# Kernel optimization log

Hardware: AMD Instinct MI355X
Metric: run time of the kernel (lower is better)

## Reference

```python
import jax, jax.numpy as jnp
import numpy as np

NUM_HEADS = 16
WINDOW = 256


def setup_inputs() -> dict:
    key = jax.random.key(0)
    ks = jax.random.split(key, 9)
    B, S, E = 2, 2048, 1024
    sc = 1.0 / np.sqrt(E)
    return {
        "x": jax.random.normal(ks[0], (B, S, E), dtype=jnp.float32),
        "Wq": jax.random.normal(ks[1], (E, E), dtype=jnp.float32) * sc,
        "bq": jnp.zeros((E,), dtype=jnp.float32),
        "Wk": jax.random.normal(ks[2], (E, E), dtype=jnp.float32) * sc,
        "bk": jnp.zeros((E,), dtype=jnp.float32),
        "Wv": jax.random.normal(ks[3], (E, E), dtype=jnp.float32) * sc,
        "bv": jnp.zeros((E,), dtype=jnp.float32),
        "Wo": jax.random.normal(ks[4], (E, E), dtype=jnp.float32) * sc,
        "bo": jnp.zeros((E,), dtype=jnp.float32),
    }


def reference(x, Wq, bq, Wk, bk, Wv, bv, Wo, bo):
    B, S, E = x.shape
    H = NUM_HEADS
    D = E // H
    Q = (x @ Wq + bq).reshape(B, S, H, D).transpose(0, 2, 1, 3)  # [B,H,S,D]
    # Faithful to original: K is view(B, H, S, D), NOT a permute of (B,S,H,D)
    K = (x @ Wk + bk).reshape(B, H, S, D)
    V = (x @ Wv + bv).reshape(B, S, H, D).transpose(0, 2, 1, 3)  # [B,H,S,D]
    scores = jnp.einsum('bhqd,bhkd->bhqk', Q, K) / jnp.sqrt(jnp.float32(D))
    # sliding-window mask: j in [i-W, i+W)  (diag included, i+W exclusive)
    i = jnp.arange(S)[:, None]
    j = jnp.arange(S)[None, :]
    mask = (j >= i - WINDOW) & (j < i + WINDOW)  # [S,S]
    scores = jnp.where(mask, scores, -jnp.inf)
    attn = jax.nn.softmax(scores, axis=-1)
    out = jnp.einsum('bhqk,bhkd->bhqd', attn, V)  # [B,H,S,D]
    out = out.transpose(0, 2, 1, 3).reshape(B, S, E)
    return out @ Wo + bo
```

## Files before the change

kernel.cpp:

```cpp
#include <hip/hip_runtime.h>

#define S_LEN 2048
#define EMB   1024
#define HEADS 16
#define HDIM  64
#define WIN   256

typedef unsigned short u16;
typedef unsigned int   u32;
typedef float  f32x4  __attribute__((ext_vector_type(4)));
typedef __bf16 bf16x8 __attribute__((ext_vector_type(8)));
typedef unsigned short u16x4 __attribute__((ext_vector_type(4)));

typedef const __attribute__((address_space(1))) u32* gas_ptr;
typedef __attribute__((address_space(3))) u32*       las_ptr;

__device__ __forceinline__ void gload16(const void* g, void* l) {
    __builtin_amdgcn_global_load_lds((gas_ptr)g, (las_ptr)l, 16, 0, 0);
}

__device__ __forceinline__ u16 f2bf(float v) {
    u32 x = __builtin_bit_cast(u32, v);
    return (u16)((x + 0x7fffu + ((x >> 16) & 1u)) >> 16);
}
__device__ __forceinline__ u32 cvt_pk_bf16(float lo, float hi) {
    u32 r;
    asm volatile("v_cvt_pk_bf16_f32 %0, %1, %2" : "=v"(r) : "v"(lo), "v"(hi));
    return r;
}

__global__ __launch_bounds__(256)
void prep_kernel(const float* __restrict__ W0, const float* __restrict__ W1,
                 const float* __restrict__ W2, const float* __restrict__ W3,
                 u16* __restrict__ T0, u16* __restrict__ T1,
                 u16* __restrict__ T2, u16* __restrict__ T3,
                 const float* __restrict__ x, u16* __restrict__ xh, int n4)
{
    const int z = blockIdx.z;
    const int tid = threadIdx.x;

    if (z == 4) {
        int bid = blockIdx.x + 16 * blockIdx.y;
        for (int i = bid * 256 + tid; i < n4; i += 65536) {
            float4 v = reinterpret_cast<const float4*>(x)[i];
            u16x4 o;
            o[0] = f2bf(v.x); o[1] = f2bf(v.y); o[2] = f2bf(v.z); o[3] = f2bf(v.w);
            reinterpret_cast<u16x4*>(xh)[i] = o;
        }
        return;
    }

    const float* W = (z == 0) ? W0 : (z == 1) ? W1 : (z == 2) ? W2 : W3;
    u16* T = (z == 0) ? T0 : (z == 1) ? T1 : (z == 2) ? T2 : T3;

    __shared__ float Ts[64][68];
    const int k0 = blockIdx.x * 64, n0 = blockIdx.y * 64;

    int r = tid >> 2, c0 = (tid & 3) * 16;
#pragma unroll
    for (int q = 0; q < 4; ++q) {
        float4 v = *reinterpret_cast<const float4*>(W + (size_t)(k0 + r) * EMB + n0 + c0 + 4 * q);
        *reinterpret_cast<float4*>(&Ts[r][c0 + 4 * q]) = v;
    }
    __syncthreads();

    int n = tid >> 2, kk0 = (tid & 3) * 16;
    u16 hb[16];
#pragma unroll
    for (int e = 0; e < 16; ++e) hb[e] = f2bf(Ts[kk0 + e][n]);
    size_t base = (size_t)(n0 + n) * EMB + k0 + kk0;
#pragma unroll
    for (int q = 0; q < 2; ++q) {
        u32 w[4];
#pragma unroll
        for (int e = 0; e < 4; ++e)
            w[e] = (u32)hb[q * 8 + 2 * e] | ((u32)hb[q * 8 + 2 * e + 1] << 16);
        *reinterpret_cast<uint4*>(T + base + q * 8) = make_uint4(w[0], w[1], w[2], w[3]);
    }
}

template<int NFN, bool OUTBF>
__global__ __launch_bounds__(256, 3)
void mfma_gemm(const u16* __restrict__ A,
               const u16* __restrict__ B0, const u16* __restrict__ B1,
               const u16* __restrict__ B2,
               const float* __restrict__ bias0, const float* __restrict__ bias1,
               const float* __restrict__ bias2,
               float s0, float s1, float s2,
               void* __restrict__ Y0, void* __restrict__ Y1, void* __restrict__ Y2,
               int M, int N, int K)
{
    constexpr int TNB = NFN * 32;

    const int z = blockIdx.z;
    const u16*   Bt   = (z == 0) ? B0 : (z == 1) ? B1 : B2;
    const float* bias = (z == 0) ? bias0 : (z == 1) ? bias1 : bias2;
    const float  scl  = (z == 0) ? s0 : (z == 1) ? s1 : s2;
    void*        Y    = (z == 0) ? Y0 : (z == 1) ? Y1 : Y2;

    __shared__ u16 lds[(128 + TNB) * 64];
    u16* lA = lds;
    u16* lB = lds + 128 * 64;

    const int tid  = threadIdx.x;
    const int wid  = tid >> 6, lane = tid & 63;
    const int wr   = wid >> 1, wc = wid & 1;
    const int lr   = lane & 15, lg = lane >> 4;
    const int l7   = lr & 7;
    const int bm   = blockIdx.y * 128, bn = blockIdx.x * TNB;

    const int crow = lane >> 3;
    const int cgrp = (lane & 7) ^ crow;

    f32x4 acc[4][NFN];
#pragma unroll
    for (int i = 0; i < 4; ++i)
#pragma unroll
        for (int j = 0; j < NFN; ++j) acc[i][j] = (f32x4)0.0f;

    for (int k0 = 0; k0 < K; k0 += 64) {
#pragma unroll
        for (int q = 0; q < 4; ++q) {
            int ch = wid * 4 + q;
            gload16(A + (size_t)(bm + ch * 8 + crow) * K + k0 + cgrp * 8,
                    lA + ch * 512);
        }
#pragma unroll
        for (int q = 0; q < TNB / 32; ++q) {
            int ch = wid * (TNB / 32) + q;
            gload16(Bt + (size_t)(bn + ch * 8 + crow) * K + k0 + cgrp * 8,
                    lB + ch * 512);
        }
        __syncthreads();

#pragma unroll
        for (int ks = 0; ks < 2; ++ks) {
            const int gsw = ((ks * 4 + lg) ^ l7) << 3;
            bf16x8 a0[4], b0[NFN];
#pragma unroll
            for (int mf = 0; mf < 4; ++mf)
                a0[mf] = *reinterpret_cast<const bf16x8*>(
                    lA + (wr * 64 + mf * 16 + lr) * 64 + gsw);
#pragma unroll
            for (int nf = 0; nf < NFN; ++nf)
                b0[nf] = *reinterpret_cast<const bf16x8*>(
                    lB + (wc * NFN * 16 + nf * 16 + lr) * 64 + gsw);
#pragma unroll
            for (int mf = 0; mf < 4; ++mf)
#pragma unroll
                for (int nf = 0; nf < NFN; ++nf)
                    acc[mf][nf] = __builtin_amdgcn_mfma_f32_16x16x32_bf16(
                        a0[mf], b0[nf], acc[mf][nf], 0, 0, 0);
        }
        __syncthreads();
    }

#pragma unroll
    for (int nf = 0; nf < NFN; ++nf) {
        int col = bn + wc * NFN * 16 + nf * 16 + lr;
        float bs = bias[col];
#pragma unroll
        for (int mf = 0; mf < 4; ++mf) {
#pragma unroll
            for (int r = 0; r < 4; ++r) {
                int row = bm + wr * 64 + mf * 16 + lg * 4 + r;
                float val = (acc[mf][nf][r] + bs) * scl;
                if (OUTBF)
                    ((u16*)Y)[(size_t)row * N + col] = f2bf(val);
                else
                    ((float*)Y)[(size_t)row * N + col] = val;
            }
        }
    }
}

__global__ __launch_bounds__(512, 4)
void attn_mfma_kernel(const u16* __restrict__ Qb, const u16* __restrict__ Kb,
                      const u16* __restrict__ Vb, u16* __restrict__ AOh)
{
    __shared__ u16 Ks[2][64 * 64];
    __shared__ u16 Vt[2][64 * 64];
    __shared__ u16 Ps[8 * 16 * 64];

    constexpr float L2E = 1.44269504f;

    const int nwg = gridDim.x * gridDim.y * gridDim.z;
    int n  = blockIdx.x + gridDim.x * (blockIdx.y + gridDim.y * blockIdx.z);
    int sw = (n & 7) * (nwg >> 3) + (n >> 3);
    const int qb = sw & 15;
    const int h  = (sw >> 4) & 15;
    const int b  = sw >> 8;

    const int i0  = qb * 128;
    const int tid = threadIdx.x;
    const int wid = tid >> 6, lane = tid & 63;
    const int lr  = lane & 15, lg = lane >> 4;
    const int l7  = lr & 7;

    const u16* Kh = Kb + (size_t)b * S_LEN * EMB + (size_t)h * S_LEN * HDIM;

    bf16x8 qa[2];
    {
        const u16* qp = Qb + ((size_t)(b * S_LEN + i0 + wid * 16 + lr)) * EMB
                        + h * HDIM + lg * 8;
        qa[0] = *reinterpret_cast<const bf16x8*>(qp);
        qa[1] = *reinterpret_cast<const bf16x8*>(qp + 32);
    }

    float m2 = -1e30f, l = 0.0f;
    f32x4 o[4];
#pragma unroll
    for (int nf = 0; nf < 4; ++nf) o[nf] = (f32x4)0.0f;

    const int tlo = (2 * qb < 4) ? 0 : 2 * qb - 4;
    const int thi = (2 * qb + 5 > 31) ? 31 : 2 * qb + 5;
    const int qg  = i0 + wid * 16 + lr;

    const int kj   = lane >> 3;
    const int kgsw = (lane & 7) ^ kj;

    const int vjp = (tid & 31) * 2, vdc = tid >> 5;
    const u16* Vh = Vb + (size_t)b * S_LEN * EMB + h * HDIM;

    uint2 vr0 = *reinterpret_cast<const uint2*>(Vh + (size_t)(tlo * 64 + vjp) * EMB + vdc * 4);
    uint2 vr1 = *reinterpret_cast<const uint2*>(Vh + (size_t)(tlo * 64 + vjp + 1) * EMB + vdc * 4);
    gload16(Kh + (size_t)(tlo * 64 + wid * 8 + kj) * HDIM + kgsw * 8,
            Ks[0] + wid * 512);

    int cur = 0;
    for (int t = tlo; t <= thi; ++t) {
        {
            const u16* e0 = reinterpret_cast<const u16*>(&vr0);
            const u16* e1 = reinterpret_cast<const u16*>(&vr1);
            int jg = vjp >> 3, jl = vjp & 7;
#pragma unroll
            for (int e = 0; e < 4; ++e) {
                int d = vdc * 4 + e;
                u32 w = (u32)e0[e] | ((u32)e1[e] << 16);
                *reinterpret_cast<u32*>(Vt[cur] + d * 64 + ((jg ^ (d & 7)) << 3) + jl) = w;
            }
        }
        __syncthreads();

        if (t < thi) {
            gload16(Kh + (size_t)((t + 1) * 64 + wid * 8 + kj) * HDIM + kgsw * 8,
                    Ks[cur ^ 1] + wid * 512);
            vr0 = *reinterpret_cast<const uint2*>(Vh + (size_t)((t + 1) * 64 + vjp) * EMB + vdc * 4);
            vr1 = *reinterpret_cast<const uint2*>(Vh + (size_t)((t + 1) * 64 + vjp + 1) * EMB + vdc * 4);
        }

        f32x4 s[4];
#pragma unroll
        for (int nf = 0; nf < 4; ++nf) s[nf] = (f32x4)0.0f;
#pragma unroll
        for (int ks = 0; ks < 2; ++ks) {
            int cg = (ks * 4 + lg) ^ l7;
#pragma unroll
            for (int nf = 0; nf < 4; ++nf) {
                bf16x8 kf = *reinterpret_cast<const bf16x8*>(
                    Ks[cur] + (nf * 16 + lr) * 64 + (cg << 3));
                s[nf] = __builtin_amdgcn_mfma_f32_16x16x32_bf16(kf, qa[ks], s[nf], 0, 0, 0);
            }
        }

        if (t <= 2 * qb - 3 || t >= 2 * qb + 4) {
            int klo = qg - WIN, khi = qg + WIN;
#pragma unroll
            for (int nf = 0; nf < 4; ++nf) {
#pragma unroll
                for (int r = 0; r < 4; ++r) {
                    int kg = t * 64 + nf * 16 + lg * 4 + r;
                    bool ok = (kg >= klo) && (kg < khi);
                    s[nf][r] = ok ? s[nf][r] : -1e30f;
                }
            }
        }

        float tmax = s[0][0];
#pragma unroll
        for (int nf = 0; nf < 4; ++nf)
#pragma unroll
            for (int r = 0; r < 4; ++r) tmax = fmaxf(tmax, s[nf][r]);
        tmax = fmaxf(tmax, __shfl_xor(tmax, 16));
        tmax = fmaxf(tmax, __shfl_xor(tmax, 32));
        float tmax2 = tmax * L2E;

        bool need = tmax2 > m2 + 12.0f;
        if (__any(need)) {
            float mn2 = fmaxf(m2, tmax2);
            float sc = __builtin_amdgcn_exp2f(m2 - mn2);
            m2 = mn2;
            l *= sc;
#pragma unroll
            for (int r = 0; r < 4; ++r) {
                float scr = __shfl(sc, lg * 4 + r);
#pragma unroll
                for (int nf = 0; nf < 4; ++nf) o[nf][r] *= scr;
            }
        }

        float ps = 0.0f;
#pragma unroll
        for (int nf = 0; nf < 4; ++nf) {
            float p0 = __builtin_amdgcn_exp2f(fmaf(s[nf][0], L2E, -m2));
            float p1 = __builtin_amdgcn_exp2f(fmaf(s[nf][1], L2E, -m2));
            float p2 = __builtin_amdgcn_exp2f(fmaf(s[nf][2], L2E, -m2));
            float p3 = __builtin_amdgcn_exp2f(fmaf(s[nf][3], L2E, -m2));
            ps += (p0 + p1) + (p2 + p3);
            u32 pk0 = cvt_pk_bf16(p0, p1);
            u32 pk1 = cvt_pk_bf16(p2, p3);
            int idx16 = wid * 1024 + lr * 64 +
                        (((nf * 2 + (lg >> 1)) ^ l7) << 3) + (lg & 1) * 4;
            *reinterpret_cast<uint2*>(Ps + idx16) = make_uint2(pk0, pk1);
        }
        ps += __shfl_xor(ps, 16);
        ps += __shfl_xor(ps, 32);
        l += ps;

#pragma unroll
        for (int ks = 0; ks < 2; ++ks) {
            int cg = (ks * 4 + lg) ^ l7;
            bf16x8 pf = *reinterpret_cast<const bf16x8*>(
                Ps + wid * 1024 + lr * 64 + (cg << 3));
#pragma unroll
            for (int nf = 0; nf < 4; ++nf) {
                bf16x8 vf = *reinterpret_cast<const bf16x8*>(
                    Vt[cur] + (nf * 16 + lr) * 64 + (cg << 3));
                o[nf] = __builtin_amdgcn_mfma_f32_16x16x32_bf16(pf, vf, o[nf], 0, 0, 0);
            }
        }
        cur ^= 1;
    }

    float inv = 1.0f / l;
#pragma unroll
    for (int r = 0; r < 4; ++r) {
        float invr = __shfl(inv, lg * 4 + r);
#pragma unroll
        for (int nf = 0; nf < 4; ++nf) {
            size_t idx = ((size_t)(b * S_LEN + i0 + wid * 16 + lg * 4 + r)) * EMB
                         + h * HDIM + nf * 16 + lr;
            AOh[idx] = f2bf(o[nf][r] * invr);
        }
    }
}

extern "C" void kernel_launch(void* const* d_in, const int* in_sizes, int n_in,
                              void* d_out, int out_size, void* d_ws, size_t ws_size,
                              hipStream_t stream)
{
    (void)n_in; (void)out_size; (void)ws_size;
    const float* x  = (const float*)d_in[0];
    const float* Wq = (const float*)d_in[1];
    const float* bq = (const float*)d_in[2];
    const float* Wk = (const float*)d_in[3];
    const float* bk = (const float*)d_in[4];
    const float* Wv = (const float*)d_in[5];
    const float* bv = (const float*)d_in[6];
    const float* Wo = (const float*)d_in[7];
    const float* bo = (const float*)d_in[8];
    float* out = (float*)d_out;

    const int B = in_sizes[0] / (S_LEN * EMB);
    const int M = B * S_LEN;

    u16* xh  = (u16*)d_ws;
    u16* WtQ = xh  + (size_t)M * EMB;
    u16* WtK = WtQ + (size_t)EMB * EMB;
    u16* WtV = WtK + (size_t)EMB * EMB;
    u16* WtO = WtV + (size_t)EMB * EMB;
    u16* Qb  = WtO + (size_t)EMB * EMB;
    u16* Kb  = Qb + (size_t)M * EMB;
    u16* Vb  = Kb + (size_t)M * EMB;
    u16* AOh = Vb + (size_t)M * EMB;

    int n4 = M * EMB / 4;
    dim3 gt(EMB / 64, EMB / 64, 5);
    prep_kernel<<<gt, 256, 0, stream>>>(Wq, Wk, Wv, Wo, WtQ, WtK, WtV, WtO,
                                        x, xh, n4);

    dim3 g1(EMB / 128, M / 128, 3);
    mfma_gemm<4, true><<<g1, 256, 0, stream>>>(
        xh, WtQ, WtK, WtV, bq, bk, bv, 0.125f, 1.0f, 1.0f,
        Qb, Kb, Vb, M, EMB, EMB);

    dim3 g2(S_LEN / 128, HEADS, B);
    attn_mfma_kernel<<<g2, 512, 0, stream>>>(Qb, Kb, Vb, AOh);

    dim3 g3(EMB / 64, M / 128, 1);
    mfma_gemm<2, false><<<g3, 256, 0, stream>>>(
        AOh, WtO, WtO, WtO, bo, bo, bo, 1.0f, 1.0f, 1.0f,
        out, out, out, M, EMB, EMB);
}
```

Baseline: 87.77 us.

## Widen QKV GEMM tile to 128x256 and process key tiles in pairs in attention

The QKV projection GEMM now uses a 128x256 output tile with 8 N-fragments per wave and an occupancy hint of 2, instead of 128x128 with a hint of 3. This raises A-tile reuse and MFMA density per LDS load but uses more registers and LDS. The attention kernel now stages two 64-key tiles per barrier using doubled K/V LDS buffers, which halves the number of __syncthreads and lengthens prefetch distance. The output GEMM is specialized into its own non-template kernel without behaviour change. The tile count is always even (6 or 10), so the pairing is valid.

```diff
diff --git a/kernel.cpp b/kernel.cpp
--- a/kernel.cpp
+++ b/kernel.cpp
@@ -79,24 +79,104 @@
     }
 }
 
-template<int NFN, bool OUTBF>
-__global__ __launch_bounds__(256, 3)
-void mfma_gemm(const u16* __restrict__ A,
-               const u16* __restrict__ B0, const u16* __restrict__ B1,
-               const u16* __restrict__ B2,
-               const float* __restrict__ bias0, const float* __restrict__ bias1,
-               const float* __restrict__ bias2,
-               float s0, float s1, float s2,
-               void* __restrict__ Y0, void* __restrict__ Y1, void* __restrict__ Y2,
-               int M, int N, int K)
+__global__ __launch_bounds__(256, 2)
+void mfma_gemm_qkv(const u16* __restrict__ A,
+                   const u16* __restrict__ B0, const u16* __restrict__ B1,
+                   const u16* __restrict__ B2,
+                   const float* __restrict__ bias0, const float* __restrict__ bias1,
+                   const float* __restrict__ bias2,
+                   float s0, float s1, float s2,
+                   u16* __restrict__ Y0, u16* __restrict__ Y1, u16* __restrict__ Y2,
+                   int M, int N, int K)
 {
-    constexpr int TNB = NFN * 32;
-
     const int z = blockIdx.z;
     const u16*   Bt   = (z == 0) ? B0 : (z == 1) ? B1 : B2;
     const float* bias = (z == 0) ? bias0 : (z == 1) ? bias1 : bias2;
     const float  scl  = (z == 0) ? s0 : (z == 1) ? s1 : s2;
-    void*        Y    = (z == 0) ? Y0 : (z == 1) ? Y1 : Y2;
+    u16*         Y    = (z == 0) ? Y0 : (z == 1) ? Y1 : Y2;
+
+    __shared__ u16 lds[(128 + 256) * 64];
+    u16* lA = lds;
+    u16* lB = lds + 128 * 64;
+
+    const int tid  = threadIdx.x;
+    const int wid  = tid >> 6, lane = tid & 63;
+    const int wr   = wid >> 1, wc = wid & 1;
+    const int lr   = lane & 15, lg = lane >> 4;
+    const int l7   = lr & 7;
+    const int bm   = blockIdx.y * 128, bn = blockIdx.x * 256;
+
+    const int crow = lane >> 3;
+    const int cgrp = (lane & 7) ^ crow;
+
+    f32x4 acc[4][8];
+#pragma unroll
+    for (int i = 0; i < 4; ++i)
+#pragma unroll
+        for (int j = 0; j < 8; ++j) acc[i][j] = (f32x4)0.0f;
+
+    for (int k0 = 0; k0 < K; k0 += 64) {
+#pragma unroll
+        for (int q = 0; q < 4; ++q) {
+            int ch = wid * 4 + q;
+            gload16(A + (size_t)(bm + ch * 8 + crow) * K + k0 + cgrp * 8,
+                    lA + ch * 512);
+        }
+#pragma unroll
+        for (int q = 0; q < 8; ++q) {
+            int ch = wid * 8 + q;
+            gload16(Bt + (size_t)(bn + ch * 8 + crow) * K + k0 + cgrp * 8,
+                    lB + ch * 512);
+        }
+        __syncthreads();
+
+#pragma unroll
+        for (int ks = 0; ks < 2; ++ks) {
+            const int gsw = ((ks * 4 + lg) ^ l7) << 3;
+            bf16x8 a0[4];
+#pragma unroll
+            for (int mf = 0; mf < 4; ++mf)
+                a0[mf] = *reinterpret_cast<const bf16x8*>(
+                    lA + (wr * 64 + mf * 16 + lr) * 64 + gsw);
+#pragma unroll
+            for (int half = 0; half < 2; ++half) {
+                bf16x8 b0[4];
+#pragma unroll
+                for (int j = 0; j < 4; ++j)
+                    b0[j] = *reinterpret_cast<const bf16x8*>(
+                        lB + (wc * 128 + (half * 4 + j) * 16 + lr) * 64 + gsw);
+#pragma unroll
+                for (int mf = 0; mf < 4; ++mf)
+#pragma unroll
+                    for (int j = 0; j < 4; ++j)
+                        acc[mf][half * 4 + j] = __builtin_amdgcn_mfma_f32_16x16x32_bf16(
+                            a0[mf], b0[j], acc[mf][half * 4 + j], 0, 0, 0);
+            }
+        }
+        __syncthreads();
+    }
+
+#pragma unroll
+    for (int nf = 0; nf < 8; ++nf) {
+        int col = bn + wc * 128 + nf * 16 + lr;
+        float bs = bias[col];
+#pragma unroll
+        for (int mf = 0; mf < 4; ++mf) {
+#pragma unroll
+            for (int r = 0; r < 4; ++r) {
+                int row = bm + wr * 64 + mf * 16 + lg * 4 + r;
+                Y[(size_t)row * N + col] = f2bf((acc[mf][nf][r] + bs) * scl);
+            }
+        }
+    }
+}
+
+__global__ __launch_bounds__(256, 3)
+void mfma_gemm_o(const u16* __restrict__ A, const u16* __restrict__ Bt,
+                 const float* __restrict__ bias, float* __restrict__ Y,
+                 int M, int N, int K)
+{
+    constexpr int TNB = 64;
 
     __shared__ u16 lds[(128 + TNB) * 64];
     u16* lA = lds;
@@ -112,11 +192,11 @@
     const int crow = lane >> 3;
     const int cgrp = (lane & 7) ^ crow;
 
-    f32x4 acc[4][NFN];
+    f32x4 acc[4][2];
 #pragma unroll
     for (int i = 0; i < 4; ++i)
 #pragma unroll
-        for (int j = 0; j < NFN; ++j) acc[i][j] = (f32x4)0.0f;
+        for (int j = 0; j < 2; ++j) acc[i][j] = (f32x4)0.0f;
 
     for (int k0 = 0; k0 < K; k0 += 64) {
 #pragma unroll
@@ -126,8 +206,8 @@
                     lA + ch * 512);
         }
 #pragma unroll
-        for (int q = 0; q < TNB / 32; ++q) {
-            int ch = wid * (TNB / 32) + q;
+        for (int q = 0; q < 2; ++q) {
+            int ch = wid * 2 + q;
             gload16(Bt + (size_t)(bn + ch * 8 + crow) * K + k0 + cgrp * 8,
                     lB + ch * 512);
         }
@@ -136,19 +216,19 @@
 #pragma unroll
         for (int ks = 0; ks < 2; ++ks) {
             const int gsw = ((ks * 4 + lg) ^ l7) << 3;
-            bf16x8 a0[4], b0[NFN];
+            bf16x8 a0[4], b0[2];
 #pragma unroll
             for (int mf = 0; mf < 4; ++mf)
                 a0[mf] = *reinterpret_cast<const bf16x8*>(
                     lA + (wr * 64 + mf * 16 + lr) * 64 + gsw);
 #pragma unroll
-            for (int nf = 0; nf < NFN; ++nf)
+            for (int nf = 0; nf < 2; ++nf)
                 b0[nf] = *reinterpret_cast<const bf16x8*>(
-                    lB + (wc * NFN * 16 + nf * 16 + lr) * 64 + gsw);
+                    lB + (wc * 32 + nf * 16 + lr) * 64 + gsw);
 #pragma unroll
             for (int mf = 0; mf < 4; ++mf)
 #pragma unroll
-                for (int nf = 0; nf < NFN; ++nf)
+                for (int nf = 0; nf < 2; ++nf)
                     acc[mf][nf] = __builtin_amdgcn_mfma_f32_16x16x32_bf16(
                         a0[mf], b0[nf], acc[mf][nf], 0, 0, 0);
         }
@@ -156,19 +236,15 @@
     }
 
 #pragma unroll
-    for (int nf = 0; nf < NFN; ++nf) {
-        int col = bn + wc * NFN * 16 + nf * 16 + lr;
+    for (int nf = 0; nf < 2; ++nf) {
+        int col = bn + wc * 32 + nf * 16 + lr;
         float bs = bias[col];
 #pragma unroll
         for (int mf = 0; mf < 4; ++mf) {
 #pragma unroll
             for (int r = 0; r < 4; ++r) {
                 int row = bm + wr * 64 + mf * 16 + lg * 4 + r;
-                float val = (acc[mf][nf][r] + bs) * scl;
-                if (OUTBF)
-                    ((u16*)Y)[(size_t)row * N + col] = f2bf(val);
-                else
-                    ((float*)Y)[(size_t)row * N + col] = val;
+                Y[(size_t)row * N + col] = acc[mf][nf][r] + bs;
             }
         }
     }
@@ -178,8 +254,8 @@
 void attn_mfma_kernel(const u16* __restrict__ Qb, const u16* __restrict__ Kb,
                       const u16* __restrict__ Vb, u16* __restrict__ AOh)
 {
-    __shared__ u16 Ks[2][64 * 64];
-    __shared__ u16 Vt[2][64 * 64];
+    __shared__ u16 Ks[2][2][64 * 64];
+    __shared__ u16 Vt[2][2][64 * 64];
     __shared__ u16 Ps[8 * 16 * 64];
 
     constexpr float L2E = 1.44269504f;
@@ -198,6 +274,7 @@
     const int l7  = lr & 7;
 
     const u16* Kh = Kb + (size_t)b * S_LEN * EMB + (size_t)h * S_LEN * HDIM;
+    const u16* Vh = Vb + (size_t)b * S_LEN * EMB + h * HDIM;
 
     bf16x8 qa[2];
     {
@@ -214,122 +291,140 @@
 
     const int tlo = (2 * qb < 4) ? 0 : 2 * qb - 4;
     const int thi = (2 * qb + 5 > 31) ? 31 : 2 * qb + 5;
+    const int np  = (thi - tlo + 1) >> 1;
     const int qg  = i0 + wid * 16 + lr;
 
     const int kj   = lane >> 3;
     const int kgsw = (lane & 7) ^ kj;
-
     const int vjp = (tid & 31) * 2, vdc = tid >> 5;
-    const u16* Vh = Vb + (size_t)b * S_LEN * EMB + h * HDIM;
-
-    uint2 vr0 = *reinterpret_cast<const uint2*>(Vh + (size_t)(tlo * 64 + vjp) * EMB + vdc * 4);
-    uint2 vr1 = *reinterpret_cast<const uint2*>(Vh + (size_t)(tlo * 64 + vjp + 1) * EMB + vdc * 4);
+
+    uint2 vr[2][2];
     gload16(Kh + (size_t)(tlo * 64 + wid * 8 + kj) * HDIM + kgsw * 8,
-            Ks[0] + wid * 512);
-
-    int cur = 0;
-    for (int t = tlo; t <= thi; ++t) {
-        {
-            const u16* e0 = reinterpret_cast<const u16*>(&vr0);
-            const u16* e1 = reinterpret_cast<const u16*>(&vr1);
+            Ks[0][0] + wid * 512);
+    gload16(Kh + (size_t)((tlo + 1) * 64 + wid * 8 + kj) * HDIM + kgsw * 8,
+            Ks[0][1] + wid * 512);
+    vr[0][0] = *reinterpret_cast<const uint2*>(Vh + (size_t)(tlo * 64 + vjp) * EMB + vdc * 4);
+    vr[0][1] = *reinterpret_cast<const uint2*>(Vh + (size_t)(tlo * 64 + vjp + 1) * EMB + vdc * 4);
+    vr[1][0] = *reinterpret_cast<const uint2*>(Vh + (size_t)((tlo + 1) * 64 + vjp) * EMB + vdc * 4);
+    vr[1][1] = *reinterpret_cast<const uint2*>(Vh + (size_t)((tlo + 1) * 64 + vjp + 1) * EMB + vdc * 4);
+
+    for (int p = 0; p < np; ++p) {
+        const int t0  = tlo + 2 * p;
+        const int buf = p & 1;
+
+#pragma unroll
+        for (int ss = 0; ss < 2; ++ss) {
+            const u16* e0 = reinterpret_cast<const u16*>(&vr[ss][0]);
+            const u16* e1 = reinterpret_cast<const u16*>(&vr[ss][1]);
             int jg = vjp >> 3, jl = vjp & 7;
 #pragma unroll
             for (int e = 0; e < 4; ++e) {
                 int d = vdc * 4 + e;
                 u32 w = (u32)e0[e] | ((u32)e1[e] << 16);
-                *reinterpret_cast<u32*>(Vt[cur] + d * 64 + ((jg ^ (d & 7)) << 3) + jl) = w;
+                *reinterpret_cast<u32*>(Vt[buf][ss] + d * 64 + ((jg ^ (d & 7)) << 3) + jl) = w;
             }
         }
         __syncthreads();
 
-        if (t < thi) {
-            gload16(Kh + (size_t)((t + 1) * 64 + wid * 8 + kj) * HDIM + kgsw * 8,
-                    Ks[cur ^ 1] + wid * 512);
-            vr0 = *reinterpret_cast<const uint2*>(Vh + (size_t)((t + 1) * 64 + vjp) * EMB + vdc * 4);
-            vr1 = *reinterpret_cast<const uint2*>(Vh + (size_t)((t + 1) * 64 + vjp + 1) * EMB + vdc * 4);
-        }
-
-        f32x4 s[4];
-#pragma unroll
-        for (int nf = 0; nf < 4; ++nf) s[nf] = (f32x4)0.0f;
-#pragma unroll
-        for (int ks = 0; ks < 2; ++ks) {
-            int cg = (ks * 4 + lg) ^ l7;
+        if (p + 1 < np) {
+            int tn = t0 + 2;
+            gload16(Kh + (size_t)(tn * 64 + wid * 8 + kj) * HDIM + kgsw * 8,
+                    Ks[buf ^ 1][0] + wid * 512);
+            gload16(Kh + (size_t)((tn + 1) * 64 + wid * 8 + kj) * HDIM + kgsw * 8,
+                    Ks[buf ^ 1][1] + wid * 512);
+            vr[0][0] = *reinterpret_cast<const uint2*>(Vh + (size_t)(tn * 64 + vjp) * EMB + vdc * 4);
+            vr[0][1] = *reinterpret_cast<const uint2*>(Vh + (size_t)(tn * 64 + vjp + 1) * EMB + vdc * 4);
+            vr[1][0] = *reinterpret_cast<const uint2*>(Vh + (size_t)((tn + 1) * 64 + vjp) * EMB + vdc * 4);
+            vr[1][1] = *reinterpret_cast<const uint2*>(Vh + (size_t)((tn + 1) * 64 + vjp + 1) * EMB + vdc * 4);
+        }
+
+#pragma unroll
+        for (int ss = 0; ss < 2; ++ss) {
+            const int t = t0 + ss;
+            const u16* KsT = Ks[buf][ss];
+            const u16* VtT = Vt[buf][ss];
+
+            f32x4 s[4];
+#pragma unroll
+            for (int nf = 0; nf < 4; ++nf) s[nf] = (f32x4)0.0f;
+#pragma unroll
+            for (int ks = 0; ks < 2; ++ks) {
+                int cg = (ks * 4 + lg) ^ l7;
+#pragma unroll
+                for (int nf = 0; nf < 4; ++nf) {
+                    bf16x8 kf = *reinterpret_cast<const bf16x8*>(
+                        KsT + (nf * 16 + lr) * 64 + (cg << 3));
+                    s[nf] = __builtin_amdgcn_mfma_f32_16x16x32_bf16(kf, qa[ks], s[nf], 0, 0, 0);
+                }
+            }
+
+            if (t <= 2 * qb - 3 || t >= 2 * qb + 4) {
+                int klo = qg - WIN, khi = qg + WIN;
+#pragma unroll
+                for (int nf = 0; nf < 4; ++nf) {
+#pragma unroll
+                    for (int r = 0; r < 4; ++r) {
+                        int kg = t * 64 + nf * 16 + lg * 4 + r;
+                        bool ok = (kg >= klo) && (kg < khi);
+                        s[nf][r] = ok ? s[nf][r] : -1e30f;
+                    }
+                }
+            }
+
+            float tmax = s[0][0];
+#pragma unroll
+            for (int nf = 0; nf < 4; ++nf)
+#pragma unroll
+                for (int r = 0; r < 4; ++r) tmax = fmaxf(tmax, s[nf][r]);
+            tmax = fmaxf(tmax, __shfl_xor(tmax, 16));
+            tmax = fmaxf(tmax, __shfl_xor(tmax, 32));
+            float tmax2 = tmax * L2E;
+
+            bool need = tmax2 > m2 + 12.0f;
+            if (__any(need)) {
+                float mn2 = fmaxf(m2, tmax2);
+                float sc = __builtin_amdgcn_exp2f(m2 - mn2);
+                m2 = mn2;
+                l *= sc;
+#pragma unroll
+                for (int r = 0; r < 4; ++r) {
+                    float scr = __shfl(sc, lg * 4 + r);
+#pragma unroll
+                    for (int nf = 0; nf < 4; ++nf) o[nf][r] *= scr;
+                }
+            }
+
+            float ps = 0.0f;
 #pragma unroll
             for (int nf = 0; nf < 4; ++nf) {
-                bf16x8 kf = *reinterpret_cast<const bf16x8*>(
-                    Ks[cur] + (nf * 16 + lr) * 64 + (cg << 3));
-                s[nf] = __builtin_amdgcn_mfma_f32_16x16x32_bf16(kf, qa[ks], s[nf], 0, 0, 0);
-            }
-        }
-
-        if (t <= 2 * qb - 3 || t >= 2 * qb + 4) {
-            int klo = qg - WIN, khi = qg + WIN;
-#pragma unroll
-            for (int nf = 0; nf < 4; ++nf) {
-#pragma unroll
-                for (int r = 0; r < 4; ++r) {
-                    int kg = t * 64 + nf * 16 + lg * 4 + r;
-                    bool ok = (kg >= klo) && (kg < khi);
-                    s[nf][r] = ok ? s[nf][r] : -1e30f;
+                float p0 = __builtin_amdgcn_exp2f(fmaf(s[nf][0], L2E, -m2));
+                float p1 = __builtin_amdgcn_exp2f(fmaf(s[nf][1], L2E, -m2));
+                float p2 = __builtin_amdgcn_exp2f(fmaf(s[nf][2], L2E, -m2));
+                float p3 = __builtin_amdgcn_exp2f(fmaf(s[nf][3], L2E, -m2));
+                ps += (p0 + p1) + (p2 + p3);
+                u32 pk0 = cvt_pk_bf16(p0, p1);
+                u32 pk1 = cvt_pk_bf16(p2, p3);
+                int idx16 = wid * 1024 + lr * 64 +
+                            (((nf * 2 + (lg >> 1)) ^ l7) << 3) + (lg & 1) * 4;
+                *reinterpret_cast<uint2*>(Ps + idx16) = make_uint2(pk0, pk1);
+            }
+            ps += __shfl_xor(ps, 16);
+            ps += __shfl_xor(ps, 32);
+            l += ps;
+
+#pragma unroll
+            for (int ks = 0; ks < 2; ++ks) {
+                int cg = (ks * 4 + lg) ^ l7;
+                bf16x8 pf = *reinterpret_cast<const bf16x8*>(
+                    Ps + wid * 1024 + lr * 64 + (cg << 3));
+#pragma unroll
+                for (int nf = 0; nf < 4; ++nf) {
+                    bf16x8 vf = *reinterpret_cast<const bf16x8*>(
+                        VtT + (nf * 16 + lr) * 64 + (cg << 3));
+                    o[nf] = __builtin_amdgcn_mfma_f32_16x16x32_bf16(pf, vf, o[nf], 0, 0, 0);
                 }
             }
         }
-
-        float tmax = s[0][0];
-#pragma unroll
-        for (int nf = 0; nf < 4; ++nf)
-#pragma unroll
-            for (int r = 0; r < 4; ++r) tmax = fmaxf(tmax, s[nf][r]);
-        tmax = fmaxf(tmax, __shfl_xor(tmax, 16));
-        tmax = fmaxf(tmax, __shfl_xor(tmax, 32));
-        float tmax2 = tmax * L2E;
-
-        bool need = tmax2 > m2 + 12.0f;
-        if (__any(need)) {
-            float mn2 = fmaxf(m2, tmax2);
-            float sc = __builtin_amdgcn_exp2f(m2 - mn2);
-            m2 = mn2;
-            l *= sc;
-#pragma unroll
-            for (int r = 0; r < 4; ++r) {
-                float scr = __shfl(sc, lg * 4 + r);
-#pragma unroll
-                for (int nf = 0; nf < 4; ++nf) o[nf][r] *= scr;
-            }
-        }
-
-        float ps = 0.0f;
-#pragma unroll
-        for (int nf = 0; nf < 4; ++nf) {
-            float p0 = __builtin_amdgcn_exp2f(fmaf(s[nf][0], L2E, -m2));
-            float p1 = __builtin_amdgcn_exp2f(fmaf(s[nf][1], L2E, -m2));
-            float p2 = __builtin_amdgcn_exp2f(fmaf(s[nf][2], L2E, -m2));
-            float p3 = __builtin_amdgcn_exp2f(fmaf(s[nf][3], L2E, -m2));
-            ps += (p0 + p1) + (p2 + p3);
-            u32 pk0 = cvt_pk_bf16(p0, p1);
-            u32 pk1 = cvt_pk_bf16(p2, p3);
-            int idx16 = wid * 1024 + lr * 64 +
-                        (((nf * 2 + (lg >> 1)) ^ l7) << 3) + (lg & 1) * 4;
-            *reinterpret_cast<uint2*>(Ps + idx16) = make_uint2(pk0, pk1);
-        }
-        ps += __shfl_xor(ps, 16);
-        ps += __shfl_xor(ps, 32);
-        l += ps;
-
-#pragma unroll
-        for (int ks = 0; ks < 2; ++ks) {
-            int cg = (ks * 4 + lg) ^ l7;
-            bf16x8 pf = *reinterpret_cast<const bf16x8*>(
-                Ps + wid * 1024 + lr * 64 + (cg << 3));
-#pragma unroll
-            for (int nf = 0; nf < 4; ++nf) {
-                bf16x8 vf = *reinterpret_cast<const bf16x8*>(
-                    Vt[cur] + (nf * 16 + lr) * 64 + (cg << 3));
-                o[nf] = __builtin_amdgcn_mfma_f32_16x16x32_bf16(pf, vf, o[nf], 0, 0, 0);
-            }
-        }
-        cur ^= 1;
     }
 
     float inv = 1.0f / l;
@@ -379,8 +474,8 @@
     prep_kernel<<<gt, 256, 0, stream>>>(Wq, Wk, Wv, Wo, WtQ, WtK, WtV, WtO,
                                         x, xh, n4);
 
-    dim3 g1(EMB / 128, M / 128, 3);
-    mfma_gemm<4, true><<<g1, 256, 0, stream>>>(
+    dim3 g1(EMB / 256, M / 128, 3);
+    mfma_gemm_qkv<<<g1, 256, 0, stream>>>(
         xh, WtQ, WtK, WtV, bq, bk, bv, 0.125f, 1.0f, 1.0f,
         Qb, Kb, Vb, M, EMB, EMB);
 
@@ -388,7 +483,5 @@
     attn_mfma_kernel<<<g2, 512, 0, stream>>>(Qb, Kb, Vb, AOh);
 
     dim3 g3(EMB / 64, M / 128, 1);
-    mfma_gemm<2, false><<<g3, 256, 0, stream>>>(
-        AOh, WtO, WtO, WtO, bo, bo, bo, 1.0f, 1.0f, 1.0f,
-        out, out, out, M, EMB, EMB);
-}
+    mfma_gemm_o<<<g3, 256, 0, stream>>>(AOh, WtO, bo, out, M, EMB, EMB);
+}
```

Result: no change. 88.56 us (+0.9%).

## Halve attention block to 4 waves, each handling 32 query rows

Applied to the files above, without the earlier changes.

The attention kernel now launches 256 threads instead of 512. Each wave processes two 16-row query tiles and reuses every K and V fragment it loads from shared memory for both tiles. K and V tile loading is redistributed across fewer threads, with wider V loads and two K chunks per wave. This roughly doubles accumulator and score registers per wave and lowers the number of waves per block, which risks reduced occupancy and less latency hiding.

```diff
diff --git a/kernel.cpp b/kernel.cpp
--- a/kernel.cpp
+++ b/kernel.cpp
@@ -174,13 +174,13 @@
     }
 }
 
-__global__ __launch_bounds__(512, 4)
+__global__ __launch_bounds__(256, 2)
 void attn_mfma_kernel(const u16* __restrict__ Qb, const u16* __restrict__ Kb,
                       const u16* __restrict__ Vb, u16* __restrict__ AOh)
 {
     __shared__ u16 Ks[2][64 * 64];
     __shared__ u16 Vt[2][64 * 64];
-    __shared__ u16 Ps[8 * 16 * 64];
+    __shared__ u16 Ps[4 * 2048];
 
     constexpr float L2E = 1.44269504f;
 
@@ -198,34 +198,42 @@
     const int l7  = lr & 7;
 
     const u16* Kh = Kb + (size_t)b * S_LEN * EMB + (size_t)h * S_LEN * HDIM;
-
-    bf16x8 qa[2];
-    {
-        const u16* qp = Qb + ((size_t)(b * S_LEN + i0 + wid * 16 + lr)) * EMB
+    const u16* Vh = Vb + (size_t)b * S_LEN * EMB + h * HDIM;
+
+    bf16x8 qa[2][2];
+#pragma unroll
+    for (int hh = 0; hh < 2; ++hh) {
+        const u16* qp = Qb + ((size_t)(b * S_LEN + i0 + wid * 32 + hh * 16 + lr)) * EMB
                         + h * HDIM + lg * 8;
-        qa[0] = *reinterpret_cast<const bf16x8*>(qp);
-        qa[1] = *reinterpret_cast<const bf16x8*>(qp + 32);
-    }
-
-    float m2 = -1e30f, l = 0.0f;
-    f32x4 o[4];
-#pragma unroll
-    for (int nf = 0; nf < 4; ++nf) o[nf] = (f32x4)0.0f;
+        qa[hh][0] = *reinterpret_cast<const bf16x8*>(qp);
+        qa[hh][1] = *reinterpret_cast<const bf16x8*>(qp + 32);
+    }
+
+    float m2[2] = {-1e30f, -1e30f}, l[2] = {0.0f, 0.0f};
+    f32x4 o[2][4];
+#pragma unroll
+    for (int hh = 0; hh < 2; ++hh)
+#pragma unroll
+        for (int nf = 0; nf < 4; ++nf) o[hh][nf] = (f32x4)0.0f;
 
     const int tlo = (2 * qb < 4) ? 0 : 2 * qb - 4;
     const int thi = (2 * qb + 5 > 31) ? 31 : 2 * qb + 5;
-    const int qg  = i0 + wid * 16 + lr;
+    int qg[2];
+    qg[0] = i0 + wid * 32 + lr;
+    qg[1] = qg[0] + 16;
 
     const int kj   = lane >> 3;
     const int kgsw = (lane & 7) ^ kj;
-
     const int vjp = (tid & 31) * 2, vdc = tid >> 5;
-    const u16* Vh = Vb + (size_t)b * S_LEN * EMB + h * HDIM;
-
-    uint2 vr0 = *reinterpret_cast<const uint2*>(Vh + (size_t)(tlo * 64 + vjp) * EMB + vdc * 4);
-    uint2 vr1 = *reinterpret_cast<const uint2*>(Vh + (size_t)(tlo * 64 + vjp + 1) * EMB + vdc * 4);
-    gload16(Kh + (size_t)(tlo * 64 + wid * 8 + kj) * HDIM + kgsw * 8,
-            Ks[0] + wid * 512);
+
+    uint4 vr0 = *reinterpret_cast<const uint4*>(Vh + (size_t)(tlo * 64 + vjp) * EMB + vdc * 8);
+    uint4 vr1 = *reinterpret_cast<const uint4*>(Vh + (size_t)(tlo * 64 + vjp + 1) * EMB + vdc * 8);
+#pragma unroll
+    for (int q = 0; q < 2; ++q) {
+        int ch = wid * 2 + q;
+        gload16(Kh + (size_t)(tlo * 64 + ch * 8 + kj) * HDIM + kgsw * 8,
+                Ks[0] + ch * 512);
+    }
 
     int cur = 0;
     for (int t = tlo; t <= thi; ++t) {
@@ -234,8 +242,8 @@
             const u16* e1 = reinterpret_cast<const u16*>(&vr1);
             int jg = vjp >> 3, jl = vjp & 7;
 #pragma unroll
-            for (int e = 0; e < 4; ++e) {
-                int d = vdc * 4 + e;
+            for (int e = 0; e < 8; ++e) {
+                int d = vdc * 8 + e;
                 u32 w = (u32)e0[e] | ((u32)e1[e] << 16);
                 *reinterpret_cast<u32*>(Vt[cur] + d * 64 + ((jg ^ (d & 7)) << 3) + jl) = w;
             }
@@ -243,15 +251,21 @@
         __syncthreads();
 
         if (t < thi) {
-            gload16(Kh + (size_t)((t + 1) * 64 + wid * 8 + kj) * HDIM + kgsw * 8,
-                    Ks[cur ^ 1] + wid * 512);
-            vr0 = *reinterpret_cast<const uint2*>(Vh + (size_t)((t + 1) * 64 + vjp) * EMB + vdc * 4);
-            vr1 = *reinterpret_cast<const uint2*>(Vh + (size_t)((t + 1) * 64 + vjp + 1) * EMB + vdc * 4);
-        }
-
-        f32x4 s[4];
-#pragma unroll
-        for (int nf = 0; nf < 4; ++nf) s[nf] = (f32x4)0.0f;
+#pragma unroll
+            for (int q = 0; q < 2; ++q) {
+                int ch = wid * 2 + q;
+                gload16(Kh + (size_t)((t + 1) * 64 + ch * 8 + kj) * HDIM + kgsw * 8,
+                        Ks[cur ^ 1] + ch * 512);
+            }
+            vr0 = *reinterpret_cast<const uint4*>(Vh + (size_t)((t + 1) * 64 + vjp) * EMB + vdc * 8);
+            vr1 = *reinterpret_cast<const uint4*>(Vh + (size_t)((t + 1) * 64 + vjp + 1) * EMB + vdc * 8);
+        }
+
+        f32x4 s[2][4];
+#pragma unroll
+        for (int hh = 0; hh < 2; ++hh)
+#pragma unroll
+            for (int nf = 0; nf < 4; ++nf) s[hh][nf] = (f32x4)0.0f;
 #pragma unroll
         for (int ks = 0; ks < 2; ++ks) {
             int cg = (ks * 4 + lg) ^ l7;
@@ -259,88 +273,113 @@
             for (int nf = 0; nf < 4; ++nf) {
                 bf16x8 kf = *reinterpret_cast<const bf16x8*>(
                     Ks[cur] + (nf * 16 + lr) * 64 + (cg << 3));
-                s[nf] = __builtin_amdgcn_mfma_f32_16x16x32_bf16(kf, qa[ks], s[nf], 0, 0, 0);
+                s[0][nf] = __builtin_amdgcn_mfma_f32_16x16x32_bf16(kf, qa[0][ks], s[0][nf], 0, 0, 0);
+                s[1][nf] = __builtin_amdgcn_mfma_f32_16x16x32_bf16(kf, qa[1][ks], s[1][nf], 0, 0, 0);
             }
         }
 
         if (t <= 2 * qb - 3 || t >= 2 * qb + 4) {
-            int klo = qg - WIN, khi = qg + WIN;
+#pragma unroll
+            for (int hh = 0; hh < 2; ++hh) {
+                int klo = qg[hh] - WIN, khi = qg[hh] + WIN;
+#pragma unroll
+                for (int nf = 0; nf < 4; ++nf) {
+#pragma unroll
+                    for (int r = 0; r < 4; ++r) {
+                        int kg = t * 64 + nf * 16 + lg * 4 + r;
+                        bool ok = (kg >= klo) && (kg < khi);
+                        s[hh][nf][r] = ok ? s[hh][nf][r] : -1e30f;
+                    }
+                }
+            }
+        }
+
+        float tmax2[2];
+#pragma unroll
+        for (int hh = 0; hh < 2; ++hh) {
+            float tmax = s[hh][0][0];
+#pragma unroll
+            for (int nf = 0; nf < 4; ++nf)
+#pragma unroll
+                for (int r = 0; r < 4; ++r) tmax = fmaxf(tmax, s[hh][nf][r]);
+            tmax = fmaxf(tmax, __shfl_xor(tmax, 16));
+            tmax = fmaxf(tmax, __shfl_xor(tmax, 32));
+            tmax2[hh] = tmax * L2E;
+        }
+
+        bool need = (tmax2[0] > m2[0] + 12.0f) || (tmax2[1] > m2[1] + 12.0f);
+        if (__any(need)) {
+            float sc[2];
+#pragma unroll
+            for (int hh = 0; hh < 2; ++hh) {
+                float mn2 = fmaxf(m2[hh], tmax2[hh]);
+                sc[hh] = __builtin_amdgcn_exp2f(m2[hh] - mn2);
+                m2[hh] = mn2;
+                l[hh] *= sc[hh];
+            }
+#pragma unroll
+            for (int r = 0; r < 4; ++r) {
+                float scr0 = __shfl(sc[0], lg * 4 + r);
+                float scr1 = __shfl(sc[1], lg * 4 + r);
+#pragma unroll
+                for (int nf = 0; nf < 4; ++nf) {
+                    o[0][nf][r] *= scr0;
+                    o[1][nf][r] *= scr1;
+                }
+            }
+        }
+
+#pragma unroll
+        for (int hh = 0; hh < 2; ++hh) {
+            float ps = 0.0f;
 #pragma unroll
             for (int nf = 0; nf < 4; ++nf) {
-#pragma unroll
-                for (int r = 0; r < 4; ++r) {
-                    int kg = t * 64 + nf * 16 + lg * 4 + r;
-                    bool ok = (kg >= klo) && (kg < khi);
-                    s[nf][r] = ok ? s[nf][r] : -1e30f;
-                }
-            }
-        }
-
-        float tmax = s[0][0];
-#pragma unroll
-        for (int nf = 0; nf < 4; ++nf)
-#pragma unroll
-            for (int r = 0; r < 4; ++r) tmax = fmaxf(tmax, s[nf][r]);
-        tmax = fmaxf(tmax, __shfl_xor(tmax, 16));
-        tmax = fmaxf(tmax, __shfl_xor(tmax, 32));
-        float tmax2 = tmax * L2E;
-
-        bool need = tmax2 > m2 + 12.0f;
-        if (__any(need)) {
-            float mn2 = fmaxf(m2, tmax2);
-            float sc = __builtin_amdgcn_exp2f(m2 - mn2);
-            m2 = mn2;
-            l *= sc;
-#pragma unroll
-            for (int r = 0; r < 4; ++r) {
-                float scr = __shfl(sc, lg * 4 + r);
-#pragma unroll
-                for (int nf = 0; nf < 4; ++nf) o[nf][r] *= scr;
-            }
-        }
-
-        float ps = 0.0f;
-#pragma unroll
-        for (int nf = 0; nf < 4; ++nf) {
-            float p0 = __builtin_amdgcn_exp2f(fmaf(s[nf][0], L2E, -m2));
-            float p1 = __builtin_amdgcn_exp2f(fmaf(s[nf][1], L2E, -m2));
-            float p2 = __builtin_amdgcn_exp2f(fmaf(s[nf][2], L2E, -m2));
-            float p3 = __builtin_amdgcn_exp2f(fmaf(s[nf][3], L2E, -m2));
-            ps += (p0 + p1) + (p2 + p3);
-            u32 pk0 = cvt_pk_bf16(p0, p1);
-            u32 pk1 = cvt_pk_bf16(p2, p3);
-            int idx16 = wid * 1024 + lr * 64 +
-                        (((nf * 2 + (lg >> 1)) ^ l7) << 3) + (lg & 1) * 4;
-            *reinterpret_cast<uint2*>(Ps + idx16) = make_uint2(pk0, pk1);
-        }
-        ps += __shfl_xor(ps, 16);
-        ps += __shfl_xor(ps, 32);
-        l += ps;
+                float p0 = __builtin_amdgcn_exp2f(fmaf(s[hh][nf][0], L2E, -m2[hh]));
+                float p1 = __builtin_amdgcn_exp2f(fmaf(s[hh][nf][1], L2E, -m2[hh]));
+                float p2 = __builtin_amdgcn_exp2f(fmaf(s[hh][nf][2], L2E, -m2[hh]));
+                float p3 = __builtin_amdgcn_exp2f(fmaf(s[hh][nf][3], L2E, -m2[hh]));
+                ps += (p0 + p1) + (p2 + p3);
+                u32 pk0 = cvt_pk_bf16(p0, p1);
+                u32 pk1 = cvt_pk_bf16(p2, p3);
+                int idx16 = wid * 2048 + hh * 1024 + lr * 64 +
+                            (((nf * 2 + (lg >> 1)) ^ l7) << 3) + (lg & 1) * 4;
+                *reinterpret_cast<uint2*>(Ps + idx16) = make_uint2(pk0, pk1);
+            }
+            ps += __shfl_xor(ps, 16);
+            ps += __shfl_xor(ps, 32);
+            l[hh] += ps;
+        }
 
 #pragma unroll
         for (int ks = 0; ks < 2; ++ks) {
             int cg = (ks * 4 + lg) ^ l7;
-            bf16x8 pf = *reinterpret_cast<const bf16x8*>(
-                Ps + wid * 1024 + lr * 64 + (cg << 3));
+            bf16x8 pf0 = *reinterpret_cast<const bf16x8*>(
+                Ps + wid * 2048 + lr * 64 + (cg << 3));
+            bf16x8 pf1 = *reinterpret_cast<const bf16x8*>(
+                Ps + wid * 2048 + 1024 + lr * 64 + (cg << 3));
 #pragma unroll
             for (int nf = 0; nf < 4; ++nf) {
                 bf16x8 vf = *reinterpret_cast<const bf16x8*>(
                     Vt[cur] + (nf * 16 + lr) * 64 + (cg << 3));
-                o[nf] = __builtin_amdgcn_mfma_f32_16x16x32_bf16(pf, vf, o[nf], 0, 0, 0);
+                o[0][nf] = __builtin_amdgcn_mfma_f32_16x16x32_bf16(pf0, vf, o[0][nf], 0, 0, 0);
+                o[1][nf] = __builtin_amdgcn_mfma_f32_16x16x32_bf16(pf1, vf, o[1][nf], 0, 0, 0);
             }
         }
         cur ^= 1;
     }
 
-    float inv = 1.0f / l;
-#pragma unroll
-    for (int r = 0; r < 4; ++r) {
-        float invr = __shfl(inv, lg * 4 + r);
-#pragma unroll
-        for (int nf = 0; nf < 4; ++nf) {
-            size_t idx = ((size_t)(b * S_LEN + i0 + wid * 16 + lg * 4 + r)) * EMB
-                         + h * HDIM + nf * 16 + lr;
-            AOh[idx] = f2bf(o[nf][r] * invr);
+#pragma unroll
+    for (int hh = 0; hh < 2; ++hh) {
+        float inv = 1.0f / l[hh];
+#pragma unroll
+        for (int r = 0; r < 4; ++r) {
+            float invr = __shfl(inv, lg * 4 + r);
+#pragma unroll
+            for (int nf = 0; nf < 4; ++nf) {
+                size_t idx = ((size_t)(b * S_LEN + i0 + wid * 32 + hh * 16 + lg * 4 + r)) * EMB
+                             + h * HDIM + nf * 16 + lr;
+                AOh[idx] = f2bf(o[hh][nf][r] * invr);
+            }
         }
     }
 }
@@ -385,7 +424,7 @@
         Qb, Kb, Vb, M, EMB, EMB);
 
     dim3 g2(S_LEN / 128, HEADS, B);
-    attn_mfma_kernel<<<g2, 512, 0, stream>>>(Qb, Kb, Vb, AOh);
+    attn_mfma_kernel<<<g2, 256, 0, stream>>>(Qb, Kb, Vb, AOh);
 
     dim3 g3(EMB / 64, M / 128, 1);
     mfma_gemm<2, false><<<g3, 256, 0, stream>>>(
```

Measured after the change: 87.35 us. No clear change (-0.5%).

## Shrink attention query tile to 64 rows with 4-wave workgroups

Applied to the files above, without the earlier changes.

The attention kernel now processes 64 query rows per workgroup with 256 threads instead of 128 rows with 512 threads, doubling the grid. Each thread loads twice as many K and V elements per tile so the 64x64 K/V tiles are still fully staged, and the key-tile range and boundary-masking test are retightened to the smaller query block. This cuts wasted work on key tiles that fall entirely outside the window for part of a larger query block, and it raises the number of workgroups for better occupancy and load balance. The cost is that each K/V tile is reloaded by more workgroups, increasing global memory and L2 traffic.

```diff
diff --git a/kernel.cpp b/kernel.cpp
--- a/kernel.cpp
+++ b/kernel.cpp
@@ -174,30 +174,31 @@
     }
 }
 
-__global__ __launch_bounds__(512, 4)
+__global__ __launch_bounds__(256, 4)
 void attn_mfma_kernel(const u16* __restrict__ Qb, const u16* __restrict__ Kb,
                       const u16* __restrict__ Vb, u16* __restrict__ AOh)
 {
     __shared__ u16 Ks[2][64 * 64];
     __shared__ u16 Vt[2][64 * 64];
-    __shared__ u16 Ps[8 * 16 * 64];
+    __shared__ u16 Ps[4 * 1024];
 
     constexpr float L2E = 1.44269504f;
 
     const int nwg = gridDim.x * gridDim.y * gridDim.z;
     int n  = blockIdx.x + gridDim.x * (blockIdx.y + gridDim.y * blockIdx.z);
     int sw = (n & 7) * (nwg >> 3) + (n >> 3);
-    const int qb = sw & 15;
-    const int h  = (sw >> 4) & 15;
-    const int b  = sw >> 8;
-
-    const int i0  = qb * 128;
+    const int qb = sw & 31;
+    const int h  = (sw >> 5) & 15;
+    const int b  = sw >> 9;
+
+    const int i0  = qb * 64;
     const int tid = threadIdx.x;
     const int wid = tid >> 6, lane = tid & 63;
     const int lr  = lane & 15, lg = lane >> 4;
     const int l7  = lr & 7;
 
     const u16* Kh = Kb + (size_t)b * S_LEN * EMB + (size_t)h * S_LEN * HDIM;
+    const u16* Vh = Vb + (size_t)b * S_LEN * EMB + h * HDIM;
 
     bf16x8 qa[2];
     {
@@ -212,20 +213,22 @@
 #pragma unroll
     for (int nf = 0; nf < 4; ++nf) o[nf] = (f32x4)0.0f;
 
-    const int tlo = (2 * qb < 4) ? 0 : 2 * qb - 4;
-    const int thi = (2 * qb + 5 > 31) ? 31 : 2 * qb + 5;
+    const int tlo = (qb < 4) ? 0 : qb - 4;
+    const int thi = (qb > 27) ? 31 : qb + 4;
     const int qg  = i0 + wid * 16 + lr;
 
     const int kj   = lane >> 3;
     const int kgsw = (lane & 7) ^ kj;
-
     const int vjp = (tid & 31) * 2, vdc = tid >> 5;
-    const u16* Vh = Vb + (size_t)b * S_LEN * EMB + h * HDIM;
-
-    uint2 vr0 = *reinterpret_cast<const uint2*>(Vh + (size_t)(tlo * 64 + vjp) * EMB + vdc * 4);
-    uint2 vr1 = *reinterpret_cast<const uint2*>(Vh + (size_t)(tlo * 64 + vjp + 1) * EMB + vdc * 4);
-    gload16(Kh + (size_t)(tlo * 64 + wid * 8 + kj) * HDIM + kgsw * 8,
-            Ks[0] + wid * 512);
+
+    uint4 vr0 = *reinterpret_cast<const uint4*>(Vh + (size_t)(tlo * 64 + vjp) * EMB + vdc * 8);
+    uint4 vr1 = *reinterpret_cast<const uint4*>(Vh + (size_t)(tlo * 64 + vjp + 1) * EMB + vdc * 8);
+#pragma unroll
+    for (int q = 0; q < 2; ++q) {
+        int ch = wid * 2 + q;
+        gload16(Kh + (size_t)(tlo * 64 + ch * 8 + kj) * HDIM + kgsw * 8,
+                Ks[0] + ch * 512);
+    }
 
     int cur = 0;
     for (int t = tlo; t <= thi; ++t) {
@@ -234,8 +237,8 @@
             const u16* e1 = reinterpret_cast<const u16*>(&vr1);
             int jg = vjp >> 3, jl = vjp & 7;
 #pragma unroll
-            for (int e = 0; e < 4; ++e) {
-                int d = vdc * 4 + e;
+            for (int e = 0; e < 8; ++e) {
+                int d = vdc * 8 + e;
                 u32 w = (u32)e0[e] | ((u32)e1[e] << 16);
                 *reinterpret_cast<u32*>(Vt[cur] + d * 64 + ((jg ^ (d & 7)) << 3) + jl) = w;
             }
@@ -243,10 +246,14 @@
         __syncthreads();
 
         if (t < thi) {
-            gload16(Kh + (size_t)((t + 1) * 64 + wid * 8 + kj) * HDIM + kgsw * 8,
-                    Ks[cur ^ 1] + wid * 512);
-            vr0 = *reinterpret_cast<const uint2*>(Vh + (size_t)((t + 1) * 64 + vjp) * EMB + vdc * 4);
-            vr1 = *reinterpret_cast<const uint2*>(Vh + (size_t)((t + 1) * 64 + vjp + 1) * EMB + vdc * 4);
+#pragma unroll
+            for (int q = 0; q < 2; ++q) {
+                int ch = wid * 2 + q;
+                gload16(Kh + (size_t)((t + 1) * 64 + ch * 8 + kj) * HDIM + kgsw * 8,
+                        Ks[cur ^ 1] + ch * 512);
+            }
+            vr0 = *reinterpret_cast<const uint4*>(Vh + (size_t)((t + 1) * 64 + vjp) * EMB + vdc * 8);
+            vr1 = *reinterpret_cast<const uint4*>(Vh + (size_t)((t + 1) * 64 + vjp + 1) * EMB + vdc * 8);
         }
 
         f32x4 s[4];
@@ -263,7 +270,7 @@
             }
         }
 
-        if (t <= 2 * qb - 3 || t >= 2 * qb + 4) {
+        if (t == qb - 4 || t == qb + 4) {
             int klo = qg - WIN, khi = qg + WIN;
 #pragma unroll
             for (int nf = 0; nf < 4; ++nf) {
@@ -384,8 +391,8 @@
         xh, WtQ, WtK, WtV, bq, bk, bv, 0.125f, 1.0f, 1.0f,
         Qb, Kb, Vb, M, EMB, EMB);
 
-    dim3 g2(S_LEN / 128, HEADS, B);
-    attn_mfma_kernel<<<g2, 512, 0, stream>>>(Qb, Kb, Vb, AOh);
+    dim3 g2(S_LEN / 64, HEADS, B);
+    attn_mfma_kernel<<<g2, 256, 0, stream>>>(Qb, Kb, Vb, AOh);
 
     dim3 g3(EMB / 64, M / 128, 1);
     mfma_gemm<2, false><<<g3, 256, 0, stream>>>(
```

New measurement: 85.07 us. 1.03x faster.
